# Kernel tuning notes

Measured on AMD Instinct MI355X. Metric: run time of the kernel, lower is better.

The kernel has to match this reference:

```python
import jax, jax.numpy as jnp
import numpy as np

B, T, D, H = 8, 2048, 1024, 64

def setup_inputs() -> dict:
    key = jax.random.key(0)
    ks = jax.random.split(key, 4)
    s = 1.0 / np.sqrt(D)
    return {
        "x": jax.random.normal(ks[0], (B, T, D), dtype=jnp.float32),
        "Wk": jax.random.normal(ks[1], (D, H), dtype=jnp.float32) * s,
        "bk": jnp.zeros((H,), dtype=jnp.float32),
        "Wq": jax.random.normal(ks[2], (D, H), dtype=jnp.float32) * s,
        "bq": jnp.zeros((H,), dtype=jnp.float32),
        "Wv": jax.random.normal(ks[3], (D, H), dtype=jnp.float32) * s,
        "bv": jnp.zeros((H,), dtype=jnp.float32),
    }

def reference(x, Wk, bk, Wq, bq, Wv, bv):
    # Linear projections: [B, T, H]
    k = x @ Wk + bk
    q = x @ Wq + bq
    v = x @ Wv + bv
    hs = k.shape[-1]
    # Scaled scores [B, T, T]
    scores = jnp.einsum('bqh,bkh->bqk', q, k) * (1.0 / np.sqrt(hs))
    # Causal mask (tril): positions j > i get -inf
    t = x.shape[1]
    causal = jnp.tril(jnp.ones((t, t), dtype=bool))
    scores = jnp.where(causal, scores, -jnp.inf)
    attn = jax.nn.softmax(scores, axis=-1)
    # Dropout is identity in eval mode
    return jnp.einsum('bqk,bkh->bqh', attn, v)
```

## Files before the change

kernel.cpp:

```cpp
#include <hip/hip_runtime.h>
#include <hip/hip_bf16.h>
#include <cmath>

#define B_ 8
#define T_ 2048
#define D_ 1024
#define H_ 64

typedef __bf16 bf16x8 __attribute__((ext_vector_type(8)));
typedef __bf16 bf16x4 __attribute__((ext_vector_type(4)));
typedef float f32x4 __attribute__((ext_vector_type(4)));

#define QSCALE 0.18033688011112042f

__device__ __forceinline__ void async_copy16(const void* g, void* lds) {
  __builtin_amdgcn_global_load_lds(
      (const __attribute__((address_space(1))) unsigned int*)g,
      (__attribute__((address_space(3))) unsigned int*)lds,
      16, 0, 0);
}

__global__ __launch_bounds__(256)
void castw_kernel(const float* __restrict__ w0,
                  const float* __restrict__ w1,
                  const float* __restrict__ w2,
                  __bf16* __restrict__ Wt) {
  __shared__ float tile[64][65];
  const int mat = blockIdx.y;
  const float* w = (mat == 0) ? w0 : (mat == 1) ? w1 : w2;
  const int d0 = blockIdx.x * 64;
  const int t = threadIdx.x;
#pragma unroll
  for (int i = 0; i < 16; i++) {
    int idx = i * 256 + t;
    int dl = idx >> 6, h = idx & 63;
    tile[dl][h] = w[(size_t)(d0 + dl) * 64 + h];
  }
  __syncthreads();
  const int h = t >> 2;
  const int dc = (t & 3) * 16;
  bf16x8 o0, o1;
#pragma unroll
  for (int j = 0; j < 8; j++) {
    o0[j] = (__bf16)tile[dc + j][h];
    o1[j] = (__bf16)tile[dc + 8 + j][h];
  }
  bf16x8* dst = (bf16x8*)(Wt + (size_t)mat * 65536 + (size_t)h * 1024 + d0 + dc);
  dst[0] = o0;
  dst[1] = o1;
}

__global__ __launch_bounds__(256)
void proj_kernel(const float* __restrict__ x,
                 const __bf16* __restrict__ Wt,
                 const float* __restrict__ bq,
                 const float* __restrict__ bk,
                 const float* __restrict__ bv,
                 __bf16* __restrict__ qb,
                 __bf16* __restrict__ kb,
                 __bf16* __restrict__ vt) {
  __shared__ __align__(16) __bf16 xs[32 * 128];
  __shared__ __align__(16) __bf16 wsl[192 * 128];

  const int tid  = threadIdx.x;
  const int wv   = tid >> 6;
  const int lane = tid & 63;
  const int ln   = lane & 15;
  const int quad = lane >> 4;
  const int m0   = blockIdx.x * 32;

  f32x4 acc[6] = {};

  for (int s = 0; s < 8; s++) {
    const int k0 = s * 128;
    __syncthreads();

#pragma unroll
    for (int j = 0; j < 12; j++) {
      int i = wv * 12 + j;
      int grow = i * 4 + (lane >> 4);
      int kc = (lane & 15) ^ (grow & 15);
      const __bf16* gp = Wt + (size_t)grow * 1024 + k0 + kc * 8;
      async_copy16(gp, wsl + i * 512);
    }

#pragma unroll
    for (int u = 0; u < 2; u++)
#pragma unroll
      for (int kh = 0; kh < 2; kh++) {
        int row = (tid >> 4) + u * 16;
        int fi = (tid & 15) + kh * 16;
        float4 f = *(const float4*)(x + (size_t)(m0 + row) * D_ + k0 + fi * 4);
        bf16x4 hv;
        hv[0] = (__bf16)f.x; hv[1] = (__bf16)f.y;
        hv[2] = (__bf16)f.z; hv[3] = (__bf16)f.w;
        int ch = fi >> 1, half = fi & 1;
        *(bf16x4*)(xs + row * 128 + ((ch ^ (row & 15)) * 8) + half * 4) = hv;
      }

    __syncthreads();

#pragma unroll
    for (int ks = 0; ks < 4; ks++) {
      bf16x8 af[2];
#pragma unroll
      for (int mt = 0; mt < 2; mt++) {
        int m = mt * 16 + ln;
        af[mt] = *(const bf16x8*)(xs + m * 128 + (((ks * 4 + quad) ^ (m & 15)) * 8));
      }
#pragma unroll
      for (int nt = 0; nt < 3; nt++) {
        int col = wv * 48 + nt * 16 + ln;
        bf16x8 bf = *(const bf16x8*)(wsl + col * 128 + (((ks * 4 + quad) ^ (col & 15)) * 8));
#pragma unroll
        for (int mt = 0; mt < 2; mt++)
          acc[mt * 3 + nt] =
              __builtin_amdgcn_mfma_f32_16x16x32_bf16(af[mt], bf, acc[mt * 3 + nt], 0, 0, 0);
      }
    }
  }

#pragma unroll
  for (int nt = 0; nt < 3; nt++) {
    int idx = wv * 48 + nt * 16;
    int mat = idx >> 6;
    int h = (idx & 63) + ln;
    float bcol = ((mat == 0) ? bq : (mat == 1) ? bk : bv)[h];
#pragma unroll
    for (int mt = 0; mt < 2; mt++) {
      f32x4 a = acc[mt * 3 + nt];
      int grow0 = m0 + mt * 16 + quad * 4;
      if (mat == 0) {
#pragma unroll
        for (int r = 0; r < 4; r++)
          qb[(size_t)(grow0 + r) * 64 + h] = (__bf16)((a[r] + bcol) * QSCALE);
      } else if (mat == 1) {
#pragma unroll
        for (int r = 0; r < 4; r++)
          kb[(size_t)(grow0 + r) * 64 + h] = (__bf16)(a[r] + bcol);
      } else {
        int bb = grow0 >> 11, t0 = grow0 & 2047;
        bf16x4 pv;
#pragma unroll
        for (int r = 0; r < 4; r++)
          pv[r] = (__bf16)(a[r] + bcol);
        *(bf16x4*)(vt + (size_t)(bb * 64 + h) * T_ + t0) = pv;
      }
    }
  }
}

__global__ __launch_bounds__(256)
void attn_kernel(const __bf16* __restrict__ qb,
                 const __bf16* __restrict__ kb,
                 const __bf16* __restrict__ vt,
                 float* __restrict__ out) {
  __shared__ __align__(16) __bf16 pA[4][16][72];
  __shared__ float ml_m[4][16];
  __shared__ float ml_l[4][16];
  __shared__ float olds[4][16][64];

  const int tid   = threadIdx.x;
  const int wv    = tid >> 6;
  const int lane  = tid & 63;
  const int ln    = lane & 15;
  const int quad  = lane >> 4;
  const int b     = blockIdx.y;

  const __bf16* Q = qb + (size_t)b * T_ * 64;
  const __bf16* K = kb + (size_t)b * T_ * 64;
  const __bf16* V = vt + (size_t)b * 64 * T_;

#pragma unroll
  for (int qt = 0; qt < 2; qt++) {
    const int jq    = qt == 0 ? blockIdx.x : 127 - blockIdx.x;
    const int qbase = jq * 16;
    const int ntiles = (jq >> 2) + 1;

    bf16x8 qa0 = *(const bf16x8*)(Q + (qbase + ln) * 64 + quad * 8);
    bf16x8 qa1 = *(const bf16x8*)(Q + (qbase + ln) * 64 + 32 + quad * 8);

    f32x4 acc[4] = {};
    float m_i = -INFINITY, l_i = 0.f;

    bf16x8 kfa[4], kfb[4], vfa[4], vfb[4];
    if (wv < ntiles) {
#pragma unroll
      for (int h = 0; h < 4; h++) {
        const __bf16* kr = K + (size_t)(wv * 64 + h * 16 + ln) * 64 + quad * 8;
        kfa[h] = *(const bf16x8*)kr;
        kfb[h] = *(const bf16x8*)(kr + 32);
      }
    }

    for (int jt = wv; jt < ntiles; jt += 4) {
      const int kv0 = jt * 64;

      f32x4 s[4] = {};
#pragma unroll
      for (int h = 0; h < 4; h++) {
        s[h] = __builtin_amdgcn_mfma_f32_16x16x32_bf16(kfa[h], qa0, s[h], 0, 0, 0);
        s[h] = __builtin_amdgcn_mfma_f32_16x16x32_bf16(kfb[h], qa1, s[h], 0, 0, 0);
      }

      if (jt + 4 < ntiles) {
#pragma unroll
        for (int h = 0; h < 4; h++) {
          const __bf16* kr = K + (size_t)(kv0 + 256 + h * 16 + ln) * 64 + quad * 8;
          kfa[h] = *(const bf16x8*)kr;
          kfb[h] = *(const bf16x8*)(kr + 32);
        }
      }
#pragma unroll
      for (int nt = 0; nt < 4; nt++) {
        const __bf16* vr = V + (size_t)(nt * 16 + ln) * T_ + kv0 + quad * 8;
        vfa[nt] = *(const bf16x8*)vr;
        vfb[nt] = *(const bf16x8*)(vr + 32);
      }

      if (kv0 + 63 > qbase) {
        const int lim = qbase + ln - kv0 - quad * 4;
#pragma unroll
        for (int h = 0; h < 4; h++)
#pragma unroll
          for (int r = 0; r < 4; r++)
            if (h * 16 + r > lim) s[h][r] = -INFINITY;
      }

      float mx = s[0][0];
#pragma unroll
      for (int h = 0; h < 4; h++)
#pragma unroll
        for (int r = 0; r < 4; r++) mx = fmaxf(mx, s[h][r]);
      mx = fmaxf(mx, __shfl_xor(mx, 16));
      mx = fmaxf(mx, __shfl_xor(mx, 32));

      float mnew = fmaxf(m_i, mx);
      float alpha = __builtin_amdgcn_exp2f(m_i - mnew);
      m_i = mnew;

      float p[4][4], sm = 0.f;
#pragma unroll
      for (int h = 0; h < 4; h++)
#pragma unroll
        for (int r = 0; r < 4; r++) {
          p[h][r] = __builtin_amdgcn_exp2f(s[h][r] - mnew);
          sm += p[h][r];
        }
      sm += __shfl_xor(sm, 16);
      sm += __shfl_xor(sm, 32);
      l_i = l_i * alpha + sm;

      float ar[4];
#pragma unroll
      for (int r = 0; r < 4; r++) ar[r] = __shfl(alpha, quad * 4 + r);
#pragma unroll
      for (int nt = 0; nt < 4; nt++)
#pragma unroll
        for (int r = 0; r < 4; r++) acc[nt][r] *= ar[r];

#pragma unroll
      for (int h = 0; h < 4; h++) {
        bf16x4 pk;
#pragma unroll
        for (int r = 0; r < 4; r++) pk[r] = (__bf16)p[h][r];
        *(bf16x4*)(&pA[wv][ln][h * 16 + quad * 4]) = pk;
      }

      bf16x8 pa0 = *(const bf16x8*)(&pA[wv][ln][quad * 8]);
      bf16x8 pa1 = *(const bf16x8*)(&pA[wv][ln][32 + quad * 8]);
#pragma unroll
      for (int nt = 0; nt < 4; nt++) {
        acc[nt] = __builtin_amdgcn_mfma_f32_16x16x32_bf16(pa0, vfa[nt], acc[nt], 0, 0, 0);
        acc[nt] = __builtin_amdgcn_mfma_f32_16x16x32_bf16(pa1, vfb[nt], acc[nt], 0, 0, 0);
      }
    }

    __syncthreads();
    if (quad == 0) {
      ml_m[wv][ln] = m_i;
      ml_l[wv][ln] = l_i;
    }
    __syncthreads();

#pragma unroll
    for (int r = 0; r < 4; r++) {
      int row = quad * 4 + r;
      float mstar = fmaxf(fmaxf(ml_m[0][row], ml_m[1][row]),
                          fmaxf(ml_m[2][row], ml_m[3][row]));
      float factor = __builtin_amdgcn_exp2f(ml_m[wv][row] - mstar);
#pragma unroll
      for (int nt = 0; nt < 4; nt++)
        olds[wv][row][nt * 16 + ln] = acc[nt][r] * factor;
    }
    __syncthreads();

    {
      int row = tid >> 4;
      int h0 = (tid & 15) * 4;
      float mstar = fmaxf(fmaxf(ml_m[0][row], ml_m[1][row]),
                          fmaxf(ml_m[2][row], ml_m[3][row]));
      float ltot = 0.f;
#pragma unroll
      for (int w = 0; w < 4; w++)
        ltot += ml_l[w][row] * __builtin_amdgcn_exp2f(ml_m[w][row] - mstar);
      float inv = 1.0f / ltot;
      float4 o = {0.f, 0.f, 0.f, 0.f};
#pragma unroll
      for (int w = 0; w < 4; w++) {
        float4 t = *(const float4*)(&olds[w][row][h0]);
        o.x += t.x; o.y += t.y; o.z += t.z; o.w += t.w;
      }
      o.x *= inv; o.y *= inv; o.z *= inv; o.w *= inv;
      *(float4*)(out + ((size_t)(b * T_ + qbase + row)) * 64 + h0) = o;
    }
  }
}

extern "C" void kernel_launch(void* const* d_in, const int* in_sizes, int n_in,
                              void* d_out, int out_size, void* d_ws, size_t ws_size,
                              hipStream_t stream) {
  const float* x  = (const float*)d_in[0];
  const float* Wk = (const float*)d_in[1];
  const float* bk = (const float*)d_in[2];
  const float* Wq = (const float*)d_in[3];
  const float* bq = (const float*)d_in[4];
  const float* Wv = (const float*)d_in[5];
  const float* bv = (const float*)d_in[6];
  float* out = (float*)d_out;

  char* ws = (char*)d_ws;
  __bf16* qb = (__bf16*)(ws);
  __bf16* kb = (__bf16*)(ws + (size_t)2 * 1024 * 1024);
  __bf16* vt = (__bf16*)(ws + (size_t)4 * 1024 * 1024);
  __bf16* Wt = (__bf16*)(ws + (size_t)6 * 1024 * 1024);

  castw_kernel<<<dim3(16, 3), 256, 0, stream>>>(Wq, Wk, Wv, Wt);
  proj_kernel<<<512, 256, 0, stream>>>(x, Wt, bq, bk, bv, qb, kb, vt);
  attn_kernel<<<dim3(64, 8), 256, 0, stream>>>(qb, kb, vt, out);
}
```

Measured before the change: 146.3 us.

## Process paired low/high query tiles together, sharing K/V fragment loads

Instead of processing the two paired query tiles (jq and 127-jq) one after another, each wave now walks the KV tiles once, computing scores for both query tiles from the same K and V fragments while the low tile is still active, then finishes the high tile alone. This aims to remove the duplicate K/V global loads for the overlapping prefix and to interleave two independent MFMA/softmax chains for more ILP. The block-to-pair mapping is also reversed for alternating batch groups to balance scheduling. The cost is roughly doubled accumulator and score register use, which may lower occupancy or cause spills.

```diff
diff --git a/kernel.cpp b/kernel.cpp
--- a/kernel.cpp
+++ b/kernel.cpp
@@ -155,7 +155,7 @@
                  const __bf16* __restrict__ kb,
                  const __bf16* __restrict__ vt,
                  float* __restrict__ out) {
-  __shared__ __align__(16) __bf16 pA[4][16][72];
+  __shared__ __align__(16) __bf16 pA[2][4][16][72];
   __shared__ float ml_m[4][16];
   __shared__ float ml_l[4][16];
   __shared__ float olds[4][16][64];
@@ -167,114 +167,226 @@
   const int quad  = lane >> 4;
   const int b     = blockIdx.y;
 
+  const int p     = ((blockIdx.y >> 2) & 1) ? blockIdx.x : 63 - blockIdx.x;
+  const int jqL   = p, jqH = 127 - p;
+  const int qbL   = jqL * 16, qbH = jqH * 16;
+  const int ntL   = (jqL >> 2) + 1;
+  const int ntH   = (jqH >> 2) + 1;
+
   const __bf16* Q = qb + (size_t)b * T_ * 64;
   const __bf16* K = kb + (size_t)b * T_ * 64;
   const __bf16* V = vt + (size_t)b * 64 * T_;
 
-#pragma unroll
-  for (int qt = 0; qt < 2; qt++) {
-    const int jq    = qt == 0 ? blockIdx.x : 127 - blockIdx.x;
-    const int qbase = jq * 16;
-    const int ntiles = (jq >> 2) + 1;
-
-    bf16x8 qa0 = *(const bf16x8*)(Q + (qbase + ln) * 64 + quad * 8);
-    bf16x8 qa1 = *(const bf16x8*)(Q + (qbase + ln) * 64 + 32 + quad * 8);
-
-    f32x4 acc[4] = {};
-    float m_i = -INFINITY, l_i = 0.f;
-
-    bf16x8 kfa[4], kfb[4], vfa[4], vfb[4];
-    if (wv < ntiles) {
+  bf16x8 qaL0 = *(const bf16x8*)(Q + (qbL + ln) * 64 + quad * 8);
+  bf16x8 qaL1 = *(const bf16x8*)(Q + (qbL + ln) * 64 + 32 + quad * 8);
+  bf16x8 qaH0 = *(const bf16x8*)(Q + (qbH + ln) * 64 + quad * 8);
+  bf16x8 qaH1 = *(const bf16x8*)(Q + (qbH + ln) * 64 + 32 + quad * 8);
+
+  f32x4 accL[4] = {}, accH[4] = {};
+  float mL = -INFINITY, lL = 0.f, mH = -INFINITY, lH = 0.f;
+
+  bf16x8 kfa[4], kfb[4], vfa[4], vfb[4];
+#pragma unroll
+  for (int h = 0; h < 4; h++) {
+    const __bf16* kr = K + (size_t)(wv * 64 + h * 16 + ln) * 64 + quad * 8;
+    kfa[h] = *(const bf16x8*)kr;
+    kfb[h] = *(const bf16x8*)(kr + 32);
+  }
+
+  int jt = wv;
+
+  for (; jt < ntL; jt += 4) {
+    const int kv0 = jt * 64;
+
+    f32x4 sH[4] = {}, sL[4] = {};
+#pragma unroll
+    for (int h = 0; h < 4; h++) {
+      sH[h] = __builtin_amdgcn_mfma_f32_16x16x32_bf16(kfa[h], qaH0, sH[h], 0, 0, 0);
+      sH[h] = __builtin_amdgcn_mfma_f32_16x16x32_bf16(kfb[h], qaH1, sH[h], 0, 0, 0);
+      sL[h] = __builtin_amdgcn_mfma_f32_16x16x32_bf16(kfa[h], qaL0, sL[h], 0, 0, 0);
+      sL[h] = __builtin_amdgcn_mfma_f32_16x16x32_bf16(kfb[h], qaL1, sL[h], 0, 0, 0);
+    }
+
+    if (jt + 4 < ntH) {
 #pragma unroll
       for (int h = 0; h < 4; h++) {
-        const __bf16* kr = K + (size_t)(wv * 64 + h * 16 + ln) * 64 + quad * 8;
+        const __bf16* kr = K + (size_t)(kv0 + 256 + h * 16 + ln) * 64 + quad * 8;
         kfa[h] = *(const bf16x8*)kr;
         kfb[h] = *(const bf16x8*)(kr + 32);
       }
     }
-
-    for (int jt = wv; jt < ntiles; jt += 4) {
-      const int kv0 = jt * 64;
-
-      f32x4 s[4] = {};
+#pragma unroll
+    for (int nt = 0; nt < 4; nt++) {
+      const __bf16* vr = V + (size_t)(nt * 16 + ln) * T_ + kv0 + quad * 8;
+      vfa[nt] = *(const bf16x8*)vr;
+      vfb[nt] = *(const bf16x8*)(vr + 32);
+    }
+
+    if (jt == ntL - 1) {
+      const int lim = qbL + ln - kv0 - quad * 4;
+#pragma unroll
+      for (int h = 0; h < 4; h++)
+#pragma unroll
+        for (int r = 0; r < 4; r++)
+          if (h * 16 + r > lim) sL[h][r] = -INFINITY;
+    }
+
+    float mxH = sH[0][0], mxL = sL[0][0];
+#pragma unroll
+    for (int h = 0; h < 4; h++)
+#pragma unroll
+      for (int r = 0; r < 4; r++) {
+        mxH = fmaxf(mxH, sH[h][r]);
+        mxL = fmaxf(mxL, sL[h][r]);
+      }
+    mxH = fmaxf(mxH, __shfl_xor(mxH, 16));
+    mxL = fmaxf(mxL, __shfl_xor(mxL, 16));
+    mxH = fmaxf(mxH, __shfl_xor(mxH, 32));
+    mxL = fmaxf(mxL, __shfl_xor(mxL, 32));
+
+    float mnH = fmaxf(mH, mxH), mnL = fmaxf(mL, mxL);
+    float alH = __builtin_amdgcn_exp2f(mH - mnH);
+    float alL = __builtin_amdgcn_exp2f(mL - mnL);
+    mH = mnH; mL = mnL;
+
+    float pH[4][4], pL[4][4], smH = 0.f, smL = 0.f;
+#pragma unroll
+    for (int h = 0; h < 4; h++)
+#pragma unroll
+      for (int r = 0; r < 4; r++) {
+        pH[h][r] = __builtin_amdgcn_exp2f(sH[h][r] - mnH);
+        pL[h][r] = __builtin_amdgcn_exp2f(sL[h][r] - mnL);
+        smH += pH[h][r];
+        smL += pL[h][r];
+      }
+    smH += __shfl_xor(smH, 16);  smL += __shfl_xor(smL, 16);
+    smH += __shfl_xor(smH, 32);  smL += __shfl_xor(smL, 32);
+    lH = lH * alH + smH;
+    lL = lL * alL + smL;
+
+    float arH[4], arL[4];
+#pragma unroll
+    for (int r = 0; r < 4; r++) {
+      arH[r] = __shfl(alH, quad * 4 + r);
+      arL[r] = __shfl(alL, quad * 4 + r);
+    }
+#pragma unroll
+    for (int nt = 0; nt < 4; nt++)
+#pragma unroll
+      for (int r = 0; r < 4; r++) {
+        accH[nt][r] *= arH[r];
+        accL[nt][r] *= arL[r];
+      }
+
+#pragma unroll
+    for (int h = 0; h < 4; h++) {
+      bf16x4 ph, pl;
+#pragma unroll
+      for (int r = 0; r < 4; r++) { ph[r] = (__bf16)pH[h][r]; pl[r] = (__bf16)pL[h][r]; }
+      *(bf16x4*)(&pA[1][wv][ln][h * 16 + quad * 4]) = ph;
+      *(bf16x4*)(&pA[0][wv][ln][h * 16 + quad * 4]) = pl;
+    }
+    bf16x8 paH0 = *(const bf16x8*)(&pA[1][wv][ln][quad * 8]);
+    bf16x8 paH1 = *(const bf16x8*)(&pA[1][wv][ln][32 + quad * 8]);
+    bf16x8 paL0 = *(const bf16x8*)(&pA[0][wv][ln][quad * 8]);
+    bf16x8 paL1 = *(const bf16x8*)(&pA[0][wv][ln][32 + quad * 8]);
+#pragma unroll
+    for (int nt = 0; nt < 4; nt++) {
+      accH[nt] = __builtin_amdgcn_mfma_f32_16x16x32_bf16(paH0, vfa[nt], accH[nt], 0, 0, 0);
+      accH[nt] = __builtin_amdgcn_mfma_f32_16x16x32_bf16(paH1, vfb[nt], accH[nt], 0, 0, 0);
+      accL[nt] = __builtin_amdgcn_mfma_f32_16x16x32_bf16(paL0, vfa[nt], accL[nt], 0, 0, 0);
+      accL[nt] = __builtin_amdgcn_mfma_f32_16x16x32_bf16(paL1, vfb[nt], accL[nt], 0, 0, 0);
+    }
+  }
+
+  for (; jt < ntH; jt += 4) {
+    const int kv0 = jt * 64;
+
+    f32x4 sH[4] = {};
+#pragma unroll
+    for (int h = 0; h < 4; h++) {
+      sH[h] = __builtin_amdgcn_mfma_f32_16x16x32_bf16(kfa[h], qaH0, sH[h], 0, 0, 0);
+      sH[h] = __builtin_amdgcn_mfma_f32_16x16x32_bf16(kfb[h], qaH1, sH[h], 0, 0, 0);
+    }
+
+    if (jt + 4 < ntH) {
 #pragma unroll
       for (int h = 0; h < 4; h++) {
-        s[h] = __builtin_amdgcn_mfma_f32_16x16x32_bf16(kfa[h], qa0, s[h], 0, 0, 0);
-        s[h] = __builtin_amdgcn_mfma_f32_16x16x32_bf16(kfb[h], qa1, s[h], 0, 0, 0);
-      }
-
-      if (jt + 4 < ntiles) {
-#pragma unroll
-        for (int h = 0; h < 4; h++) {
-          const __bf16* kr = K + (size_t)(kv0 + 256 + h * 16 + ln) * 64 + quad * 8;
-          kfa[h] = *(const bf16x8*)kr;
-          kfb[h] = *(const bf16x8*)(kr + 32);
-        }
-      }
-#pragma unroll
-      for (int nt = 0; nt < 4; nt++) {
-        const __bf16* vr = V + (size_t)(nt * 16 + ln) * T_ + kv0 + quad * 8;
-        vfa[nt] = *(const bf16x8*)vr;
-        vfb[nt] = *(const bf16x8*)(vr + 32);
-      }
-
-      if (kv0 + 63 > qbase) {
-        const int lim = qbase + ln - kv0 - quad * 4;
-#pragma unroll
-        for (int h = 0; h < 4; h++)
-#pragma unroll
-          for (int r = 0; r < 4; r++)
-            if (h * 16 + r > lim) s[h][r] = -INFINITY;
-      }
-
-      float mx = s[0][0];
+        const __bf16* kr = K + (size_t)(kv0 + 256 + h * 16 + ln) * 64 + quad * 8;
+        kfa[h] = *(const bf16x8*)kr;
+        kfb[h] = *(const bf16x8*)(kr + 32);
+      }
+    }
+#pragma unroll
+    for (int nt = 0; nt < 4; nt++) {
+      const __bf16* vr = V + (size_t)(nt * 16 + ln) * T_ + kv0 + quad * 8;
+      vfa[nt] = *(const bf16x8*)vr;
+      vfb[nt] = *(const bf16x8*)(vr + 32);
+    }
+
+    if (jt == ntH - 1) {
+      const int lim = qbH + ln - kv0 - quad * 4;
 #pragma unroll
       for (int h = 0; h < 4; h++)
 #pragma unroll
-        for (int r = 0; r < 4; r++) mx = fmaxf(mx, s[h][r]);
-      mx = fmaxf(mx, __shfl_xor(mx, 16));
-      mx = fmaxf(mx, __shfl_xor(mx, 32));
-
-      float mnew = fmaxf(m_i, mx);
-      float alpha = __builtin_amdgcn_exp2f(m_i - mnew);
-      m_i = mnew;
-
-      float p[4][4], sm = 0.f;
-#pragma unroll
-      for (int h = 0; h < 4; h++)
-#pragma unroll
-        for (int r = 0; r < 4; r++) {
-          p[h][r] = __builtin_amdgcn_exp2f(s[h][r] - mnew);
-          sm += p[h][r];
-        }
-      sm += __shfl_xor(sm, 16);
-      sm += __shfl_xor(sm, 32);
-      l_i = l_i * alpha + sm;
-
-      float ar[4];
-#pragma unroll
-      for (int r = 0; r < 4; r++) ar[r] = __shfl(alpha, quad * 4 + r);
-#pragma unroll
-      for (int nt = 0; nt < 4; nt++)
-#pragma unroll
-        for (int r = 0; r < 4; r++) acc[nt][r] *= ar[r];
-
-#pragma unroll
-      for (int h = 0; h < 4; h++) {
-        bf16x4 pk;
-#pragma unroll
-        for (int r = 0; r < 4; r++) pk[r] = (__bf16)p[h][r];
-        *(bf16x4*)(&pA[wv][ln][h * 16 + quad * 4]) = pk;
-      }
-
-      bf16x8 pa0 = *(const bf16x8*)(&pA[wv][ln][quad * 8]);
-      bf16x8 pa1 = *(const bf16x8*)(&pA[wv][ln][32 + quad * 8]);
-#pragma unroll
-      for (int nt = 0; nt < 4; nt++) {
-        acc[nt] = __builtin_amdgcn_mfma_f32_16x16x32_bf16(pa0, vfa[nt], acc[nt], 0, 0, 0);
-        acc[nt] = __builtin_amdgcn_mfma_f32_16x16x32_bf16(pa1, vfb[nt], acc[nt], 0, 0, 0);
-      }
-    }
+        for (int r = 0; r < 4; r++)
+          if (h * 16 + r > lim) sH[h][r] = -INFINITY;
+    }
+
+    float mxH = sH[0][0];
+#pragma unroll
+    for (int h = 0; h < 4; h++)
+#pragma unroll
+      for (int r = 0; r < 4; r++) mxH = fmaxf(mxH, sH[h][r]);
+    mxH = fmaxf(mxH, __shfl_xor(mxH, 16));
+    mxH = fmaxf(mxH, __shfl_xor(mxH, 32));
+
+    float mnH = fmaxf(mH, mxH);
+    float alH = __builtin_amdgcn_exp2f(mH - mnH);
+    mH = mnH;
+
+    float pH[4][4], smH = 0.f;
+#pragma unroll
+    for (int h = 0; h < 4; h++)
+#pragma unroll
+      for (int r = 0; r < 4; r++) {
+        pH[h][r] = __builtin_amdgcn_exp2f(sH[h][r] - mnH);
+        smH += pH[h][r];
+      }
+    smH += __shfl_xor(smH, 16);
+    smH += __shfl_xor(smH, 32);
+    lH = lH * alH + smH;
+
+    float arH[4];
+#pragma unroll
+    for (int r = 0; r < 4; r++) arH[r] = __shfl(alH, quad * 4 + r);
+#pragma unroll
+    for (int nt = 0; nt < 4; nt++)
+#pragma unroll
+      for (int r = 0; r < 4; r++) accH[nt][r] *= arH[r];
+
+#pragma unroll
+    for (int h = 0; h < 4; h++) {
+      bf16x4 ph;
+#pragma unroll
+      for (int r = 0; r < 4; r++) ph[r] = (__bf16)pH[h][r];
+      *(bf16x4*)(&pA[1][wv][ln][h * 16 + quad * 4]) = ph;
+    }
+    bf16x8 paH0 = *(const bf16x8*)(&pA[1][wv][ln][quad * 8]);
+    bf16x8 paH1 = *(const bf16x8*)(&pA[1][wv][ln][32 + quad * 8]);
+#pragma unroll
+    for (int nt = 0; nt < 4; nt++) {
+      accH[nt] = __builtin_amdgcn_mfma_f32_16x16x32_bf16(paH0, vfa[nt], accH[nt], 0, 0, 0);
+      accH[nt] = __builtin_amdgcn_mfma_f32_16x16x32_bf16(paH1, vfb[nt], accH[nt], 0, 0, 0);
+    }
+  }
+
+#pragma unroll
+  for (int side = 0; side < 2; side++) {
+    const float m_i = side == 0 ? mL : mH;
+    const float l_i = side == 0 ? lL : lH;
+    const f32x4* acc = side == 0 ? accL : accH;
+    const int qbase  = side == 0 ? qbL : qbH;
 
     __syncthreads();
     if (quad == 0) {
```

New measurement: 140.9 us. -3.7%, faster.
